# Kernel tuning notes

Hardware: AMD Instinct MI355X
Metric: run time of the kernel (lower is better)

Reference implementation:

```python
import jax, jax.numpy as jnp
import numpy as np


def setup_inputs() -> dict:
    key = jax.random.key(0)
    ks = jax.random.split(key, 5)
    B, Lq, Lkv, HQ, H, D, S, BS = 1, 256, 4096, 32, 2, 128, 16, 64
    q = jax.random.normal(ks[0], (B, Lq, HQ, D), jnp.float32)
    k = jax.random.normal(ks[1], (B, Lkv, H, D), jnp.float32)
    v = jax.random.normal(ks[2], (B, Lkv, H, D), jnp.float32)
    w = jax.random.uniform(ks[3], (B, Lq, HQ, S), jnp.float32)
    block_indices = jax.random.randint(ks[4], (B, Lq, H, S), 0, Lkv // BS).astype(jnp.int32)
    return {"q": q, "k": k, "v": v, "w": w, "block_indices": block_indices, "block_size": BS}


def reference(q, k, v, w, block_indices, block_size):
    # q: (B, Lq, HQ, D); k,v: (B, Lkv, H, D); w: (B, Lq, HQ, num_weights);
    # block_indices: (B, Lq, H, S) int32, entries < 0 are skipped.
    B, Lq, HQ, D = q.shape
    H = k.shape[2]
    S = block_indices.shape[-1]
    G = HQ // H  # query heads per kv head
    nb = k.shape[1] // block_size
    sm_scale = 1.0 / (D ** 0.5)  # default scale in the kernel

    # Reshape KV into blocks: (B, H, nb, BS, D)
    kb = k.reshape(B, nb, block_size, H, D).transpose(0, 3, 1, 2, 4)
    vb = v.reshape(B, nb, block_size, H, D).transpose(0, 3, 1, 2, 4)

    idx = block_indices.transpose(0, 2, 1, 3)  # (B, H, Lq, S)
    valid = idx >= 0
    idx = jnp.maximum(idx, 0)

    # Gather selected blocks per (batch, kv_head): -> (B, H, Lq, S, BS, D)
    gather = jax.vmap(jax.vmap(lambda blocks, ind: blocks[ind]))
    kg = gather(kb, idx)
    vg = gather(vb, idx)

    # Group query heads by kv head: (B, H, Lq, G, D)
    qh = q.reshape(B, Lq, H, G, D).transpose(0, 2, 1, 3, 4)

    # Per-block scores and per-block softmax over the BS keys (axis u)
    scores = jnp.einsum('bhlgd,bhlsud->bhlgsu', qh, kg) * sm_scale
    p = jax.nn.softmax(scores, axis=-1)

    # Per-(head, block) learned weight; only first S weights of w are used.
    wh = w[..., :S].reshape(B, Lq, H, G, S).transpose(0, 2, 1, 3, 4)  # (B,H,Lq,G,S)
    coef = wh * valid[:, :, :, None, :].astype(p.dtype)
    p = p * coef[..., None]

    o = jnp.einsum('bhlgsu,bhlsud->bhlgd', p, vg)  # (B, H, Lq, G, D)
    return o.transpose(0, 2, 1, 3, 4).reshape(B, Lq, HQ, D)
```

## Files before the change

### kernel.cpp

```cpp
#include <hip/hip_runtime.h>
#include <hip/hip_bf16.h>


namespace {

constexpr int kLq = 256, kHQ = 32, kH = 2, kG = 16, kD = 128, kS = 16;
constexpr int kNB = 64;
constexpr float kScaleLog2e = 0.08838834764831845f * 1.4426950408889634f;

constexpr int kKPackN = kH * kNB * 16 * 64;
constexpr int kPStr   = 72;
constexpr int kSStr   = 136;

typedef short s16x8 __attribute__((ext_vector_type(8)));
typedef float f32x4 __attribute__((ext_vector_type(4)));

union U32BF2 { unsigned int u; __hip_bfloat162 h; };
union FragU  { uint4 u; s16x8 v; };

static __device__ inline unsigned int pk_bf16(float a, float b) {
    U32BF2 z; z.h = __float22bfloat162_rn(make_float2(a, b));
    return z.u;
}

__global__ __launch_bounds__(256)
void pack_kv(const float* __restrict__ k, const float* __restrict__ v,
             uint4* __restrict__ kp, uint4* __restrict__ vp)
{
    __shared__ unsigned short S_s[32 * kSStr];

    const int bid  = blockIdx.x;
    const int isV  = bid & 1;
    const int half = (bid >> 1) & 1;
    const int blk  = (bid >> 2) & 63;
    const int h    = bid >> 8;
    const int t    = threadIdx.x;
    const int lane = t & 63, n = lane & 15, quad = lane >> 4;
    const int wv   = t >> 6;

    {
        const float* src = (isV ? v : k) +
            ((size_t)(blk * 64 + half * 32) * kH + h) * kD;
        const int r0 = t >> 5, c4 = (t & 31) << 2;
        #pragma unroll
        for (int p = 0; p < 4; ++p) {
            const int r = p * 8 + r0;
            const float4 f = *(const float4*)(src + (size_t)r * (kH * kD) + c4);
            *(unsigned int*)&S_s[r * kSStr + c4]     = pk_bf16(f.x, f.y);
            *(unsigned int*)&S_s[r * kSStr + c4 + 2] = pk_bf16(f.z, f.w);
        }
    }
    __syncthreads();

    const size_t obase = (size_t)(h * 64 + blk) * 16 * 64;
    if (!isV) {
        #pragma unroll
        for (int rep = 0; rep < 2; ++rep) {
            const int cl    = wv * 2 + rep;
            const int t_loc = cl >> 2, st = cl & 3;
            const int c     = (2 * half + t_loc) * 4 + st;
            const int u_loc = t_loc * 16 + n;
            kp[obase + (size_t)c * 64 + lane] =
                *(const uint4*)&S_s[u_loc * kSStr + st * 32 + quad * 8];
        }
    } else {
        #pragma unroll
        for (int rep = 0; rep < 2; ++rep) {
            const int dt = wv * 2 + rep;
            const int c  = dt * 2 + half;
            const int d  = dt * 16 + n;
            unsigned short s[8];
            #pragma unroll
            for (int j = 0; j < 8; ++j) s[j] = S_s[(quad * 8 + j) * kSStr + d];
            uint4 val;
            val.x = s[0] | ((unsigned)s[1] << 16);
            val.y = s[2] | ((unsigned)s[3] << 16);
            val.z = s[4] | ((unsigned)s[5] << 16);
            val.w = s[6] | ((unsigned)s[7] << 16);
            vp[obase + (size_t)c * 64 + lane] = val;
        }
    }
}

__global__ __launch_bounds__(512, 4)
void hsa_main(const float* __restrict__ q, const float* __restrict__ w,
              const int* __restrict__ bidx, const uint4* __restrict__ kp,
              const uint4* __restrict__ vp, float* __restrict__ out)
{
    __shared__ __align__(16) unsigned short P_s[2][2][kG * kPStr];
    __shared__ __align__(16) float psum[2][2][kG][4];
    __shared__ __align__(16) float Ored[kD * kG];

    const int bid  = blockIdx.x;
    const int l    = bid >> 1;
    const int h    = bid & 1;
    const int tid  = threadIdx.x;
    const int wave = tid >> 6;
    const int team = wave >> 2;
    const int tw   = wave & 3;
    const int lane = tid & 63;
    const int n    = lane & 15;
    const int quad = lane >> 4;

    s16x8 qf[4];
    {
        const float* qb = q + ((size_t)l * kHQ + h * kG + n) * kD + quad * 8;
        #pragma unroll
        for (int st = 0; st < 4; ++st) {
            const float4 f0 = *(const float4*)(qb + st * 32);
            const float4 f1 = *(const float4*)(qb + st * 32 + 4);
            union { s16x8 v; unsigned int u[4]; } z;
            z.u[0] = pk_bf16(f0.x, f0.y); z.u[1] = pk_bf16(f0.z, f0.w);
            z.u[2] = pk_bf16(f1.x, f1.y); z.u[3] = pk_bf16(f1.z, f1.w);
            qf[st] = z.v;
        }
    }

    int   base8[8];
    float wval8[8];
    #pragma unroll
    for (int j = 0; j < 8; ++j) {
        const int s  = 2 * j + team;
        const int bi = bidx[(size_t)(l * kH + h) * kS + s];
        wval8[j] = (bi < 0) ? 0.f : w[((size_t)l * kHQ + h * kG + n) * kS + s];
        base8[j] = (h * kNB + max(bi, 0)) * 1024;
    }

    FragU kreg[4], vreg[4];
    #pragma unroll
    for (int st = 0; st < 4; ++st)
        kreg[st].u = kp[base8[0] + (tw * 4 + st) * 64 + lane];
    #pragma unroll
    for (int i = 0; i < 4; ++i)
        vreg[i].u = vp[base8[0] + (tw * 4 + i) * 64 + lane];
    __builtin_amdgcn_sched_barrier(0);

    f32x4 oacc0 = {0.f, 0.f, 0.f, 0.f};
    f32x4 oacc1 = {0.f, 0.f, 0.f, 0.f};

    #pragma unroll
    for (int jp = 0; jp < 8; ++jp) {
        const int cur = jp & 1;

        f32x4 sc = {0.f, 0.f, 0.f, 0.f};
        #pragma unroll
        for (int st = 0; st < 4; ++st)
            sc = __builtin_amdgcn_mfma_f32_16x16x32_bf16(kreg[st].v, qf[st], sc, 0, 0, 0);

        float part = 0.f;
        #pragma unroll
        for (int r = 0; r < 4; ++r) {
            sc[r] = exp2f(sc[r] * kScaleLog2e);
            part += sc[r];
        }
        part += __shfl_xor(part, 16);
        part += __shfl_xor(part, 32);
        if (quad == 0) psum[cur][team][n][tw] = part;

        const unsigned long long pq =
            ((unsigned long long)pk_bf16(sc[2], sc[3]) << 32) | pk_bf16(sc[0], sc[1]);
        *(unsigned long long*)&P_s[cur][team][n * kPStr + tw * 16 + quad * 4] = pq;

        __syncthreads();

        if (jp < 7) {
            #pragma unroll
            for (int st = 0; st < 4; ++st)
                kreg[st].u = kp[base8[jp + 1] + (tw * 4 + st) * 64 + lane];
        }
        __builtin_amdgcn_sched_barrier(0);

        const float4 ps  = *(const float4*)&psum[cur][team][n][0];
        const float coef = wval8[jp] / (ps.x + ps.y + ps.z + ps.w);
        const s16x8 bf0 = *(const s16x8*)&P_s[cur][team][n * kPStr + quad * 8];
        const s16x8 bf1 = *(const s16x8*)&P_s[cur][team][n * kPStr + 32 + quad * 8];

        const f32x4 zero = {0.f, 0.f, 0.f, 0.f};
        f32x4 p0 = __builtin_amdgcn_mfma_f32_16x16x32_bf16(vreg[0].v, bf0, zero, 0, 0, 0);
        p0       = __builtin_amdgcn_mfma_f32_16x16x32_bf16(vreg[1].v, bf1, p0,   0, 0, 0);
        f32x4 p1 = __builtin_amdgcn_mfma_f32_16x16x32_bf16(vreg[2].v, bf0, zero, 0, 0, 0);
        p1       = __builtin_amdgcn_mfma_f32_16x16x32_bf16(vreg[3].v, bf1, p1,   0, 0, 0);
        #pragma unroll
        for (int r = 0; r < 4; ++r) {
            oacc0[r] = fmaf(coef, p0[r], oacc0[r]);
            oacc1[r] = fmaf(coef, p1[r], oacc1[r]);
        }

        if (jp < 7) {
            #pragma unroll
            for (int i = 0; i < 4; ++i)
                vreg[i].u = vp[base8[jp + 1] + (tw * 4 + i) * 64 + lane];
        }
        __builtin_amdgcn_sched_barrier(0);
    }

    __syncthreads();
    if (team == 1) {
        #pragma unroll
        for (int r = 0; r < 4; ++r) {
            Ored[((tw * 2 + 0) * 16 + quad * 4 + r) * 16 + n] = oacc0[r];
            Ored[((tw * 2 + 1) * 16 + quad * 4 + r) * 16 + n] = oacc1[r];
        }
    }
    __syncthreads();
    if (team == 0) {
        float* ob = out + ((size_t)l * kHQ + h * kG + n) * kD;
        const int d0 = tw * 32 + quad * 4;
        float4 v0, v1;
        #pragma unroll
        for (int r = 0; r < 4; ++r) {
            (&v0.x)[r] = oacc0[r] + Ored[(d0 + r) * 16 + n];
            (&v1.x)[r] = oacc1[r] + Ored[(d0 + 16 + r) * 16 + n];
        }
        *(float4*)(ob + d0)      = v0;
        *(float4*)(ob + d0 + 16) = v1;
    }
}

}

extern "C" void kernel_launch(void* const* d_in, const int* in_sizes, int n_in,
                              void* d_out, int out_size, void* d_ws, size_t ws_size,
                              hipStream_t stream)
{
    const float* q    = (const float*)d_in[0];
    const float* k    = (const float*)d_in[1];
    const float* v    = (const float*)d_in[2];
    const float* w    = (const float*)d_in[3];
    const int*   bidx = (const int*)d_in[4];
    float* out = (float*)d_out;

    uint4* kp = (uint4*)d_ws;
    uint4* vp = (uint4*)((char*)d_ws + (size_t)kKPackN * 16);

    pack_kv<<<dim3(512), dim3(256), 0, stream>>>(k, v, kp, vp);
    hsa_main<<<dim3(kLq * kH), dim3(512), 0, stream>>>(q, w, bidx, kp, vp, out);
}
```

Measured before the change: 91.03 us.

## Give each wave whole KV blocks to remove per-step block barriers

Before, 8 waves split each selected block's 64 keys and the D dimension and synced through shared memory at every step. Now each wave processes two whole blocks: it computes all 64 scores itself, keeps the softmax row sum in registers and reads P from a private shared-memory slice. This removes the __syncthreads from the main loop. In exchange each wave holds all 8 output tiles in registers and the eight partial outputs are combined by a tree reduction through shared memory with several barriers. K and V loads are now serialised per sub-tile, which may expose more memory latency and raise register pressure.

```diff
diff --git a/kernel.cpp b/kernel.cpp
--- a/kernel.cpp
+++ b/kernel.cpp
@@ -87,17 +87,13 @@
               const int* __restrict__ bidx, const uint4* __restrict__ kp,
               const uint4* __restrict__ vp, float* __restrict__ out)
 {
-    __shared__ __align__(16) unsigned short P_s[2][2][kG * kPStr];
-    __shared__ __align__(16) float psum[2][2][kG][4];
-    __shared__ __align__(16) float Ored[kD * kG];
+    __shared__ __align__(16) float smem[8192];
 
     const int bid  = blockIdx.x;
     const int l    = bid >> 1;
     const int h    = bid & 1;
     const int tid  = threadIdx.x;
     const int wave = tid >> 6;
-    const int team = wave >> 2;
-    const int tw   = wave & 3;
     const int lane = tid & 63;
     const int n    = lane & 15;
     const int quad = lane >> 4;
@@ -116,104 +112,147 @@
         }
     }
 
-    int   base8[8];
-    float wval8[8];
-    #pragma unroll
-    for (int j = 0; j < 8; ++j) {
-        const int s  = 2 * j + team;
+    int   base2[2];
+    float wval2[2];
+    #pragma unroll
+    for (int j = 0; j < 2; ++j) {
+        const int s  = wave * 2 + j;
         const int bi = bidx[(size_t)(l * kH + h) * kS + s];
-        wval8[j] = (bi < 0) ? 0.f : w[((size_t)l * kHQ + h * kG + n) * kS + s];
-        base8[j] = (h * kNB + max(bi, 0)) * 1024;
-    }
-
-    FragU kreg[4], vreg[4];
-    #pragma unroll
-    for (int st = 0; st < 4; ++st)
-        kreg[st].u = kp[base8[0] + (tw * 4 + st) * 64 + lane];
-    #pragma unroll
-    for (int i = 0; i < 4; ++i)
-        vreg[i].u = vp[base8[0] + (tw * 4 + i) * 64 + lane];
+        wval2[j] = (bi < 0) ? 0.f : w[((size_t)l * kHQ + h * kG + n) * kS + s];
+        base2[j] = (h * kNB + max(bi, 0)) * 1024;
+    }
+
+    unsigned short* Pw = (unsigned short*)smem + wave * (kG * kPStr);
+
+    FragU kA[4], kB[4], vr[4];
+    #pragma unroll
+    for (int st = 0; st < 4; ++st) kA[st].u = kp[base2[0] + (0 * 4 + st) * 64 + lane];
+    #pragma unroll
+    for (int st = 0; st < 4; ++st) kB[st].u = kp[base2[0] + (1 * 4 + st) * 64 + lane];
+    #pragma unroll
+    for (int i = 0; i < 4; ++i)    vr[i].u  = vp[base2[0] + i * 64 + lane];
     __builtin_amdgcn_sched_barrier(0);
 
-    f32x4 oacc0 = {0.f, 0.f, 0.f, 0.f};
-    f32x4 oacc1 = {0.f, 0.f, 0.f, 0.f};
-
-    #pragma unroll
-    for (int jp = 0; jp < 8; ++jp) {
-        const int cur = jp & 1;
-
-        f32x4 sc = {0.f, 0.f, 0.f, 0.f};
-        #pragma unroll
-        for (int st = 0; st < 4; ++st)
-            sc = __builtin_amdgcn_mfma_f32_16x16x32_bf16(kreg[st].v, qf[st], sc, 0, 0, 0);
-
+    f32x4 oacc[8];
+    #pragma unroll
+    for (int dt = 0; dt < 8; ++dt) oacc[dt] = (f32x4){0.f, 0.f, 0.f, 0.f};
+
+    #pragma unroll
+    for (int jb = 0; jb < 2; ++jb) {
         float part = 0.f;
         #pragma unroll
-        for (int r = 0; r < 4; ++r) {
-            sc[r] = exp2f(sc[r] * kScaleLog2e);
-            part += sc[r];
-        }
+        for (int t = 0; t < 4; ++t) {
+            FragU* cur = (t & 1) ? kB : kA;
+            f32x4 sc = {0.f, 0.f, 0.f, 0.f};
+            #pragma unroll
+            for (int st = 0; st < 4; ++st)
+                sc = __builtin_amdgcn_mfma_f32_16x16x32_bf16(cur[st].v, qf[st], sc, 0, 0, 0);
+
+            if (t < 2) {
+                #pragma unroll
+                for (int st = 0; st < 4; ++st)
+                    cur[st].u = kp[base2[jb] + ((t + 2) * 4 + st) * 64 + lane];
+            } else if (jb == 0) {
+                #pragma unroll
+                for (int st = 0; st < 4; ++st)
+                    cur[st].u = kp[base2[1] + ((t - 2) * 4 + st) * 64 + lane];
+            }
+            __builtin_amdgcn_sched_barrier(0);
+
+            #pragma unroll
+            for (int r = 0; r < 4; ++r) {
+                sc[r] = exp2f(sc[r] * kScaleLog2e);
+                part += sc[r];
+            }
+            const unsigned long long pq =
+                ((unsigned long long)pk_bf16(sc[2], sc[3]) << 32) | pk_bf16(sc[0], sc[1]);
+            *(unsigned long long*)&Pw[n * kPStr + t * 16 + quad * 4] = pq;
+        }
+
         part += __shfl_xor(part, 16);
         part += __shfl_xor(part, 32);
-        if (quad == 0) psum[cur][team][n][tw] = part;
-
-        const unsigned long long pq =
-            ((unsigned long long)pk_bf16(sc[2], sc[3]) << 32) | pk_bf16(sc[0], sc[1]);
-        *(unsigned long long*)&P_s[cur][team][n * kPStr + tw * 16 + quad * 4] = pq;
-
-        __syncthreads();
-
-        if (jp < 7) {
-            #pragma unroll
-            for (int st = 0; st < 4; ++st)
-                kreg[st].u = kp[base8[jp + 1] + (tw * 4 + st) * 64 + lane];
-        }
-        __builtin_amdgcn_sched_barrier(0);
-
-        const float4 ps  = *(const float4*)&psum[cur][team][n][0];
-        const float coef = wval8[jp] / (ps.x + ps.y + ps.z + ps.w);
-        const s16x8 bf0 = *(const s16x8*)&P_s[cur][team][n * kPStr + quad * 8];
-        const s16x8 bf1 = *(const s16x8*)&P_s[cur][team][n * kPStr + 32 + quad * 8];
+        const float coef = wval2[jb] / part;
+
+        const s16x8 bf0 = *(const s16x8*)&Pw[n * kPStr + quad * 8];
+        const s16x8 bf1 = *(const s16x8*)&Pw[n * kPStr + 32 + quad * 8];
 
         const f32x4 zero = {0.f, 0.f, 0.f, 0.f};
-        f32x4 p0 = __builtin_amdgcn_mfma_f32_16x16x32_bf16(vreg[0].v, bf0, zero, 0, 0, 0);
-        p0       = __builtin_amdgcn_mfma_f32_16x16x32_bf16(vreg[1].v, bf1, p0,   0, 0, 0);
-        f32x4 p1 = __builtin_amdgcn_mfma_f32_16x16x32_bf16(vreg[2].v, bf0, zero, 0, 0, 0);
-        p1       = __builtin_amdgcn_mfma_f32_16x16x32_bf16(vreg[3].v, bf1, p1,   0, 0, 0);
-        #pragma unroll
-        for (int r = 0; r < 4; ++r) {
-            oacc0[r] = fmaf(coef, p0[r], oacc0[r]);
-            oacc1[r] = fmaf(coef, p1[r], oacc1[r]);
-        }
-
-        if (jp < 7) {
-            #pragma unroll
-            for (int i = 0; i < 4; ++i)
-                vreg[i].u = vp[base8[jp + 1] + (tw * 4 + i) * 64 + lane];
-        }
-        __builtin_amdgcn_sched_barrier(0);
-    }
-
-    __syncthreads();
-    if (team == 1) {
-        #pragma unroll
-        for (int r = 0; r < 4; ++r) {
-            Ored[((tw * 2 + 0) * 16 + quad * 4 + r) * 16 + n] = oacc0[r];
-            Ored[((tw * 2 + 1) * 16 + quad * 4 + r) * 16 + n] = oacc1[r];
-        }
-    }
-    __syncthreads();
-    if (team == 0) {
+        #pragma unroll
+        for (int vg = 0; vg < 4; ++vg) {
+            const int dt0 = vg * 2;
+            f32x4 p0 = __builtin_amdgcn_mfma_f32_16x16x32_bf16(vr[0].v, bf0, zero, 0, 0, 0);
+            p0       = __builtin_amdgcn_mfma_f32_16x16x32_bf16(vr[1].v, bf1, p0,   0, 0, 0);
+            f32x4 p1 = __builtin_amdgcn_mfma_f32_16x16x32_bf16(vr[2].v, bf0, zero, 0, 0, 0);
+            p1       = __builtin_amdgcn_mfma_f32_16x16x32_bf16(vr[3].v, bf1, p1,   0, 0, 0);
+
+            if (vg < 3) {
+                #pragma unroll
+                for (int i = 0; i < 4; ++i)
+                    vr[i].u = vp[base2[jb] + ((vg + 1) * 4 + i) * 64 + lane];
+            } else if (jb == 0) {
+                #pragma unroll
+                for (int i = 0; i < 4; ++i)
+                    vr[i].u = vp[base2[1] + i * 64 + lane];
+            }
+            __builtin_amdgcn_sched_barrier(0);
+
+            #pragma unroll
+            for (int r = 0; r < 4; ++r) {
+                oacc[dt0 + 0][r] = fmaf(coef, p0[r], oacc[dt0 + 0][r]);
+                oacc[dt0 + 1][r] = fmaf(coef, p1[r], oacc[dt0 + 1][r]);
+            }
+        }
+    }
+
+    __syncthreads();
+    float* epi = smem;
+
+    if (wave >= 4) {
+        #pragma unroll
+        for (int dt = 0; dt < 8; ++dt)
+            *(f32x4*)&epi[(wave - 4) * 2048 + dt * 256 + lane * 4] = oacc[dt];
+    }
+    __syncthreads();
+    if (wave < 4) {
+        #pragma unroll
+        for (int dt = 0; dt < 8; ++dt) {
+            const f32x4 o = *(const f32x4*)&epi[wave * 2048 + dt * 256 + lane * 4];
+            #pragma unroll
+            for (int r = 0; r < 4; ++r) oacc[dt][r] += o[r];
+        }
+    }
+    __syncthreads();
+    if (wave == 2 || wave == 3) {
+        #pragma unroll
+        for (int dt = 0; dt < 8; ++dt)
+            *(f32x4*)&epi[(wave - 2) * 2048 + dt * 256 + lane * 4] = oacc[dt];
+    }
+    __syncthreads();
+    if (wave < 2) {
+        #pragma unroll
+        for (int dt = 0; dt < 8; ++dt) {
+            const f32x4 o = *(const f32x4*)&epi[wave * 2048 + dt * 256 + lane * 4];
+            #pragma unroll
+            for (int r = 0; r < 4; ++r) oacc[dt][r] += o[r];
+        }
+    }
+    __syncthreads();
+    if (wave == 1) {
+        #pragma unroll
+        for (int dt = 0; dt < 8; ++dt)
+            *(f32x4*)&epi[dt * 256 + lane * 4] = oacc[dt];
+    }
+    __syncthreads();
+    if (wave == 0) {
         float* ob = out + ((size_t)l * kHQ + h * kG + n) * kD;
-        const int d0 = tw * 32 + quad * 4;
-        float4 v0, v1;
-        #pragma unroll
-        for (int r = 0; r < 4; ++r) {
-            (&v0.x)[r] = oacc0[r] + Ored[(d0 + r) * 16 + n];
-            (&v1.x)[r] = oacc1[r] + Ored[(d0 + 16 + r) * 16 + n];
-        }
-        *(float4*)(ob + d0)      = v0;
-        *(float4*)(ob + d0 + 16) = v1;
+        #pragma unroll
+        for (int dt = 0; dt < 8; ++dt) {
+            const f32x4 o = *(const f32x4*)&epi[dt * 256 + lane * 4];
+            float4 val;
+            #pragma unroll
+            for (int r = 0; r < 4; ++r) (&val.x)[r] = oacc[dt][r] + o[r];
+            *(float4*)(ob + dt * 16 + quad * 4) = val;
+        }
     }
 }
 
```

Result: faster. 89.02 us (-2.2%).
